# Optimization experiments

Hardware: AMD Instinct MI355X
Metric: run time of the kernel (lower is better)

The kernel has to match this reference:

```python
import jax, jax.numpy as jnp
import numpy as np

DT = 0.005


def quat_product(q, r):
    # q, r: [B, 4] -> [B, 4]
    q0, q1, q2, q3 = q[:, 0], q[:, 1], q[:, 2], q[:, 3]
    r0, r1, r2, r3 = r[:, 0], r[:, 1], r[:, 2], r[:, 3]
    return jnp.stack([
        q0 * r0 - q1 * r1 - q2 * r2 - q3 * r3,
        q0 * r1 + q1 * r0 + q2 * r3 - q3 * r2,
        q0 * r2 - q1 * r3 + q2 * r0 + q3 * r1,
        q0 * r3 + q1 * r2 - q2 * r1 + q3 * r0,
    ], axis=1)


def quat_rotate(q, v):
    # q: [B, 4], v: [B, 3] -> [B, 3]
    q_conj = jnp.concatenate([q[:, :1], -q[:, 1:]], axis=1)
    v_quat = jnp.concatenate([jnp.zeros_like(v[:, :1]), v], axis=1)
    return quat_product(quat_product(q, v_quat), q_conj)[:, 1:]


def setup_inputs() -> dict:
    key = jax.random.key(0)
    ks = jax.random.split(key, 8)
    B, S, F, N = 1048576, 10, 6, 2097152
    return {
        "true_quaternions": jax.random.normal(ks[0], (B, 4), dtype=jnp.float32),
        "true_positions": jax.random.normal(ks[1], (B, 3), dtype=jnp.float32),
        "predicted_biases": jax.random.normal(ks[2], (B, 3), dtype=jnp.float32),
        "batch_X": jax.random.normal(ks[3], (B, S, F), dtype=jnp.float32),
        "positions_all": jax.random.normal(ks[4], (N, 3), dtype=jnp.float32),
        "velocities_all": jax.random.normal(ks[5], (N, 3), dtype=jnp.float32),
        "gravity_vector": jnp.array([0.0, 0.0, -9.81], dtype=jnp.float32),
        "indices": jax.random.randint(ks[6], (B,), 0, N, dtype=jnp.int64 if jax.config.jax_enable_x64 else jnp.int32),
        "sequence_length": 10,
    }


def reference(true_quaternions, true_positions, predicted_biases, batch_X,
              positions_all, velocities_all, gravity_vector, indices,
              sequence_length):
    # gather initial state: initial_index = max(idx - (seq_len - 1), 0)
    init_idx = jnp.maximum(indices - (sequence_length - 1), 0)
    p0 = positions_all[init_idx]   # [B, 3]
    v0 = velocities_all[init_idx]  # [B, 3]
    # bias-corrected acceleration from last timestep (disturbance = 0)
    acc = batch_X[:, -1, 0:3] - predicted_biases  # [B, 3]
    rotated = 0.5 * quat_rotate(true_quaternions, acc) * DT ** 2
    pred = p0 + v0 * DT + 0.5 * gravity_vector * DT ** 2 + rotated
    # Huber loss, delta = 1.0; per-sample mean over 3 coords then batch mean
    # equals elementwise mean over all B*3 elements
    d = pred - true_positions
    ad = jnp.abs(d)
    h = jnp.where(ad < 1.0, 0.5 * d * d, ad - 0.5)
    return jnp.mean(h)
```

## Files before the change

### kernel.cpp

```cpp
#include <hip/hip_runtime.h>
#include <math.h>

#define DT 0.005f
#define NTHREADS 256
#define NBLOCKS 2048
#define NBUCKET 32
#define ELEMS_PER_BLOCK 1024
#define ROUNDS 4

typedef float    fvec4 __attribute__((ext_vector_type(4)));
typedef float    fvec2 __attribute__((ext_vector_type(2)));
typedef unsigned uvec4 __attribute__((ext_vector_type(4)));
typedef float    fvec4u __attribute__((ext_vector_type(4), aligned(4)));

__device__ __forceinline__ fvec4 ntload4f(const float* p) {
    return __builtin_nontemporal_load(reinterpret_cast<const fvec4*>(p));
}
__device__ __forceinline__ fvec2 ntload2f(const float* p) {
    return __builtin_nontemporal_load(reinterpret_cast<const fvec2*>(p));
}
__device__ __forceinline__ float ntloadf(const float* p) {
    return __builtin_nontemporal_load(p);
}
__device__ __forceinline__ int ntloadi(const int* p) {
    return __builtin_nontemporal_load(p);
}
__device__ __forceinline__ uvec4 ntload4u(const unsigned* p) {
    return __builtin_nontemporal_load(reinterpret_cast<const uvec4*>(p));
}

__device__ __forceinline__ void stream_compute(
    const float* __restrict__ quat, const float* __restrict__ tpos,
    const float* __restrict__ bias, const float* __restrict__ batchX,
    int i, int SF, int last_off,
    float gx, float gy, float gz, float half_dt2,
    float& cx, float& cy, float& cz)
{
    fvec4 q = ntload4f(quat + (size_t)i * 4);
    const float* tp = tpos + (size_t)i * 3;
    float tpx = ntloadf(tp + 0), tpy = ntloadf(tp + 1), tpz = ntloadf(tp + 2);
    const float* bp = bias + (size_t)i * 3;
    float bx = ntloadf(bp + 0), by = ntloadf(bp + 1), bz = ntloadf(bp + 2);
    const float* xb = batchX + (size_t)i * SF + last_off;
    fvec2 a01 = ntload2f(xb);
    float ax = a01.x - bx;
    float ay = a01.y - by;
    float az = ntloadf(xb + 2) - bz;

    float t0 = -(q.y * ax + q.z * ay + q.w * az);
    float t1 =   q.x * ax + q.z * az - q.w * ay;
    float t2 =   q.x * ay - q.y * az + q.w * ax;
    float t3 =   q.x * az + q.y * ay - q.z * ax;
    float rx = -t0 * q.y + t1 * q.x - t2 * q.w + t3 * q.z;
    float ry = -t0 * q.z + t1 * q.w + t2 * q.x - t3 * q.y;
    float rz = -t0 * q.w - t1 * q.z + t2 * q.y + t3 * q.x;

    cx = half_dt2 * (gx + rx) - tpx;
    cy = half_dt2 * (gy + ry) - tpy;
    cz = half_dt2 * (gz + rz) - tpz;
}

__device__ __forceinline__ float huber3(float dx, float dy, float dz) {
    float adx = fabsf(dx), ady = fabsf(dy), adz = fabsf(dz);
    float h = (adx < 1.f) ? 0.5f * dx * dx : adx - 0.5f;
    h += (ady < 1.f) ? 0.5f * dy * dy : ady - 0.5f;
    h += (adz < 1.f) ? 0.5f * dz * dz : adz - 0.5f;
    return h;
}

__global__ __launch_bounds__(NTHREADS) void k1_bin(
    const float* __restrict__ quat,
    const float* __restrict__ tpos,
    const float* __restrict__ bias,
    const float* __restrict__ batchX,
    const float* __restrict__ grav,
    const int*   __restrict__ indices,
    const int*   __restrict__ seq_len_p,
    int SF, int shift,
    uvec4* __restrict__ pairs,
    int*   __restrict__ dirs)
{
    const int S = *seq_len_p;
    const int F = SF / S;
    const int last_off = (S - 1) * F;
    const float gx = grav[0], gy = grav[1], gz = grav[2];
    const float half_dt2 = 0.5f * DT * DT;

    __shared__ int   cnt[ROUNDS][4][NBUCKET];
    __shared__ int   offarr[ROUNDS][4][NBUCKET];
    __shared__ int   bstart[NBUCKET];
    __shared__ uvec4 stage[ELEMS_PER_BLOCK];

    const int tid  = threadIdx.x;
    const int wave = tid >> 6;
    const int lane = tid & 63;
    const unsigned long long ltmask = (1ull << lane) - 1ull;

    for (int k = tid; k < ROUNDS * 4 * NBUCKET; k += NTHREADS)
        ((int*)cnt)[k] = 0;
    __syncthreads();

    const int base = blockIdx.x * ELEMS_PER_BLOCK;

    int   idxv[ROUNDS], bckt[ROUNDS], rnk[ROUNDS];
    float cxv[ROUNDS], cyv[ROUNDS], czv[ROUNDS];

    #pragma unroll
    for (int r = 0; r < ROUNDS; ++r) {
        const int i = base + r * NTHREADS + tid;
        int idx = ntloadi(indices + i) - (S - 1);
        if (idx < 0) idx = 0;
        idxv[r] = idx;
        int b = idx >> shift; if (b > NBUCKET - 1) b = NBUCKET - 1;
        bckt[r] = b;

        unsigned long long mask = ~0ull;
        #pragma unroll
        for (int k = 0; k < 5; ++k) {
            unsigned long long bm = __ballot((b >> k) & 1);
            mask &= ((b >> k) & 1) ? bm : ~bm;
        }
        rnk[r] = __popcll(mask & ltmask);
        if (rnk[r] == 0) cnt[r][wave][b] = __popcll(mask);

        stream_compute(quat, tpos, bias, batchX, i, SF, last_off,
                       gx, gy, gz, half_dt2, cxv[r], cyv[r], czv[r]);
    }
    __syncthreads();

    if (tid < NBUCKET) {
        int b = tid, off = 0;
        #pragma unroll
        for (int r = 0; r < ROUNDS; ++r)
            #pragma unroll
            for (int w = 0; w < 4; ++w) {
                offarr[r][w][b] = off;
                off += cnt[r][w][b];
            }
        dirs[blockIdx.x * NBUCKET + b] = off;
        cnt[0][0][b] = off;
    }
    __syncthreads();
    if (tid == 0) {
        int s = 0;
        #pragma unroll
        for (int b = 0; b < NBUCKET; ++b) { bstart[b] = s; s += cnt[0][0][b]; }
    }
    __syncthreads();

    #pragma unroll
    for (int r = 0; r < ROUNDS; ++r) {
        int slot = bstart[bckt[r]] + offarr[r][wave][bckt[r]] + rnk[r];
        uvec4 v;
        v.x = (unsigned)idxv[r];
        v.y = __float_as_uint(cxv[r]);
        v.z = __float_as_uint(cyv[r]);
        v.w = __float_as_uint(czv[r]);
        stage[slot] = v;
    }
    __syncthreads();

    #pragma unroll
    for (int r = 0; r < ROUNDS; ++r)
        pairs[(size_t)base + r * NTHREADS + tid] = stage[r * NTHREADS + tid];
}

__global__ __launch_bounds__(NTHREADS) void k2_gather(
    const float* __restrict__ pos_all,
    const float* __restrict__ vel_all,
    const uvec4* __restrict__ pairs,
    const int*   __restrict__ dirs,
    int Nm1,
    float* __restrict__ partials)
{
    const int r = blockIdx.x & 7;
    const int j = blockIdx.x >> 3;
    const int tid = threadIdx.x;

    __shared__ int dcnt[8][NBUCKET];
    __shared__ int segSrc[8];
    __shared__ int segCum[9];
    __shared__ float wsum[NTHREADS / 64];

    {
        int s = tid >> 5, bb = tid & (NBUCKET - 1);
        dcnt[s][bb] = dirs[(j * 8 + s) * NBUCKET + bb];
    }
    __syncthreads();

    float hsum = 0.f;

    for (int phase = 0; phase < NBUCKET / 8; ++phase) {
        const int b = r + 8 * phase;

        if (tid < 8) {
            int s = tid, st = 0;
            for (int bb = 0; bb < b; ++bb) st += dcnt[s][bb];
            segSrc[s] = (j * 8 + s) * ELEMS_PER_BLOCK + st;
            segCum[s] = dcnt[s][b];
        }
        __syncthreads();
        if (tid == 0) {
            int c = 0;
            #pragma unroll
            for (int s = 0; s < 8; ++s) { int l = segCum[s]; segCum[s] = c; c += l; }
            segCum[8] = c;
        }
        __syncthreads();

        const int tot = segCum[8];
        for (int m = tid; m < tot; m += NTHREADS) {
            int s = 0;
            #pragma unroll
            for (int k = 1; k < 8; ++k) s += (m >= segCum[k]);
            uvec4 pr = ntload4u(
                reinterpret_cast<const unsigned*>(pairs + segSrc[s] + (m - segCum[s])));
            int idx = (int)pr.x;

            float px, py, pz, vx, vy, vz;
            if (idx < Nm1) {
                fvec4u pv = *reinterpret_cast<const fvec4u*>(pos_all + (size_t)idx * 3);
                fvec4u vv = *reinterpret_cast<const fvec4u*>(vel_all + (size_t)idx * 3);
                px = pv.x; py = pv.y; pz = pv.z;
                vx = vv.x; vy = vv.y; vz = vv.z;
            } else {
                const float* pp = pos_all + (size_t)idx * 3;
                const float* vp = vel_all + (size_t)idx * 3;
                px = pp[0]; py = pp[1]; pz = pp[2];
                vx = vp[0]; vy = vp[1]; vz = vp[2];
            }

            hsum += huber3(px + vx * DT + __uint_as_float(pr.y),
                           py + vy * DT + __uint_as_float(pr.z),
                           pz + vz * DT + __uint_as_float(pr.w));
        }
        __syncthreads();
    }

    for (int off = 32; off > 0; off >>= 1)
        hsum += __shfl_down(hsum, off);

    int lane = tid & 63, wid = tid >> 6;
    if (lane == 0) wsum[wid] = hsum;
    __syncthreads();
    if (tid == 0) {
        float s = 0.f;
        for (int w = 0; w < NTHREADS / 64; ++w) s += wsum[w];
        partials[blockIdx.x] = s;
    }
}

__global__ __launch_bounds__(NTHREADS) void pos_loss_partial(
    const float* __restrict__ quat,
    const float* __restrict__ tpos,
    const float* __restrict__ bias,
    const float* __restrict__ batchX,
    const float* __restrict__ pos_all,
    const float* __restrict__ vel_all,
    const float* __restrict__ grav,
    const int*   __restrict__ indices,
    const int*   __restrict__ seq_len_p,
    int B, int SF,
    float* __restrict__ partials)
{
    const int S = *seq_len_p;
    const int F = SF / S;
    const int last_off = (S - 1) * F;
    const float gx = grav[0], gy = grav[1], gz = grav[2];
    const float half_dt2 = 0.5f * DT * DT;

    float hsum = 0.f;

    for (int i = blockIdx.x * blockDim.x + threadIdx.x; i < B;
         i += gridDim.x * blockDim.x) {
        int idx = ntloadi(indices + i) - (S - 1);
        if (idx < 0) idx = 0;
        const float* pp = pos_all + (size_t)idx * 3;
        const float* vp = vel_all + (size_t)idx * 3;
        float p0x = pp[0], p0y = pp[1], p0z = pp[2];
        float v0x = vp[0], v0y = vp[1], v0z = vp[2];

        float cx, cy, cz;
        stream_compute(quat, tpos, bias, batchX, i, SF, last_off,
                       gx, gy, gz, half_dt2, cx, cy, cz);

        hsum += huber3(p0x + v0x * DT + cx,
                       p0y + v0y * DT + cy,
                       p0z + v0z * DT + cz);
    }

    for (int off = 32; off > 0; off >>= 1)
        hsum += __shfl_down(hsum, off);

    __shared__ float wsum[NTHREADS / 64];
    int lane = threadIdx.x & 63;
    int wid  = threadIdx.x >> 6;
    if (lane == 0) wsum[wid] = hsum;
    __syncthreads();
    if (threadIdx.x == 0) {
        float s = 0.f;
        for (int w = 0; w < NTHREADS / 64; ++w) s += wsum[w];
        partials[blockIdx.x] = s;
    }
}

__global__ __launch_bounds__(NTHREADS) void pos_loss_finish(
    const float* __restrict__ partials, int nb, float inv_cnt,
    float* __restrict__ out)
{
    float s = 0.f;
    for (int i = threadIdx.x; i < nb; i += NTHREADS) s += partials[i];
    for (int off = 32; off > 0; off >>= 1)
        s += __shfl_down(s, off);
    __shared__ float wsum[NTHREADS / 64];
    int lane = threadIdx.x & 63;
    int wid  = threadIdx.x >> 6;
    if (lane == 0) wsum[wid] = s;
    __syncthreads();
    if (threadIdx.x == 0) {
        float tot = 0.f;
        for (int w = 0; w < NTHREADS / 64; ++w) tot += wsum[w];
        out[0] = tot * inv_cnt;
    }
}

extern "C" void kernel_launch(void* const* d_in, const int* in_sizes, int n_in,
                              void* d_out, int out_size, void* d_ws, size_t ws_size,
                              hipStream_t stream) {
    const float* quat    = (const float*)d_in[0];
    const float* tpos    = (const float*)d_in[1];
    const float* bias    = (const float*)d_in[2];
    const float* batchX  = (const float*)d_in[3];
    const float* pos_all = (const float*)d_in[4];
    const float* vel_all = (const float*)d_in[5];
    const float* grav    = (const float*)d_in[6];
    const int*   indices = (const int*)d_in[7];
    const int*   seqlen  = (const int*)d_in[8];

    const int B  = in_sizes[0] / 4;
    const int SF = in_sizes[3] / B;
    const int N  = in_sizes[4] / 3;

    float inv_cnt = (float)(1.0 / (3.0 * (double)B));
    float* outp = (float*)d_out;

    const int nseg = B / ELEMS_PER_BLOCK;
    uvec4* pairs    = (uvec4*)d_ws;
    int*   dirs     = (int*)((char*)d_ws + (size_t)B * 16);
    float* partials = (float*)((char*)d_ws + (size_t)B * 16 +
                               (size_t)nseg * NBUCKET * 4);
    const size_t need = (size_t)B * 16 + (size_t)nseg * NBUCKET * 4 +
                        (size_t)nseg * 4 + 256;

    const bool pipe_ok = (B % (ELEMS_PER_BLOCK * 8) == 0) && (ws_size >= need) &&
                         (N > NBUCKET);

    if (pipe_ok) {
        int shift = 0;
        while (((long long)(N - 1) >> shift) >= NBUCKET) ++shift;

        k1_bin<<<nseg, NTHREADS, 0, stream>>>(
            quat, tpos, bias, batchX, grav, indices, seqlen,
            SF, shift, pairs, dirs);
        k2_gather<<<nseg, NTHREADS, 0, stream>>>(
            pos_all, vel_all, pairs, dirs, N - 1, partials);
        pos_loss_finish<<<1, NTHREADS, 0, stream>>>(
            partials, nseg, inv_cnt, outp);
    } else {
        float* fpart = (float*)d_ws;
        pos_loss_partial<<<NBLOCKS, NTHREADS, 0, stream>>>(
            quat, tpos, bias, batchX, pos_all, vel_all, grav, indices, seqlen,
            B, SF, fpart);
        pos_loss_finish<<<1, NTHREADS, 0, stream>>>(
            fpart, NBLOCKS, inv_cnt, outp);
    }
}
```

Before: 59.73 us.

## Pack binned records into 8 bytes with fp16 offsets and fuse final reduction

The intermediate per-sample record written by the binning kernel and read by the gather kernel shrinks from 16 bytes to 8. It holds a 16-bit index relative to its bucket base and three fp16 partial-position terms. This halves that round-trip traffic, but the fp16 rounding of the offsets adds error to the loss. The final partial-sum reduction is folded into the gather kernel through a cooperative grid sync when occupancy allows, removing a separate launch. The batchX load also becomes a single unaligned 4-wide load.

```diff
diff --git a/kernel.cpp b/kernel.cpp
--- a/kernel.cpp
+++ b/kernel.cpp
@@ -1,4 +1,6 @@
 #include <hip/hip_runtime.h>
+#include <hip/hip_fp16.h>
+#include <hip/hip_cooperative_groups.h>
 #include <math.h>
 
 #define DT 0.005f
@@ -8,6 +10,8 @@
 #define ELEMS_PER_BLOCK 1024
 #define ROUNDS 4
 
+namespace cg = cooperative_groups;
+
 typedef float    fvec4 __attribute__((ext_vector_type(4)));
 typedef float    fvec2 __attribute__((ext_vector_type(2)));
 typedef unsigned uvec4 __attribute__((ext_vector_type(4)));
@@ -16,17 +20,21 @@
 __device__ __forceinline__ fvec4 ntload4f(const float* p) {
     return __builtin_nontemporal_load(reinterpret_cast<const fvec4*>(p));
 }
-__device__ __forceinline__ fvec2 ntload2f(const float* p) {
-    return __builtin_nontemporal_load(reinterpret_cast<const fvec2*>(p));
-}
 __device__ __forceinline__ float ntloadf(const float* p) {
     return __builtin_nontemporal_load(p);
 }
 __device__ __forceinline__ int ntloadi(const int* p) {
     return __builtin_nontemporal_load(p);
 }
-__device__ __forceinline__ uvec4 ntload4u(const unsigned* p) {
-    return __builtin_nontemporal_load(reinterpret_cast<const uvec4*>(p));
+__device__ __forceinline__ unsigned long long ntload8(const unsigned long long* p) {
+    return __builtin_nontemporal_load(p);
+}
+
+__device__ __forceinline__ unsigned short f2h(float f) {
+    return __half_as_ushort(__float2half(f));
+}
+__device__ __forceinline__ float h2f(unsigned short u) {
+    return __half2float(__ushort_as_half(u));
 }
 
 __device__ __forceinline__ void stream_compute(
@@ -42,10 +50,10 @@
     const float* bp = bias + (size_t)i * 3;
     float bx = ntloadf(bp + 0), by = ntloadf(bp + 1), bz = ntloadf(bp + 2);
     const float* xb = batchX + (size_t)i * SF + last_off;
-    fvec2 a01 = ntload2f(xb);
-    float ax = a01.x - bx;
-    float ay = a01.y - by;
-    float az = ntloadf(xb + 2) - bz;
+    fvec4u a = *reinterpret_cast<const fvec4u*>(xb);
+    float ax = a.x - bx;
+    float ay = a.y - by;
+    float az = a.z - bz;
 
     float t0 = -(q.y * ax + q.z * ay + q.w * az);
     float t1 =   q.x * ax + q.z * az - q.w * ay;
@@ -77,7 +85,7 @@
     const int*   __restrict__ indices,
     const int*   __restrict__ seq_len_p,
     int SF, int shift,
-    uvec4* __restrict__ pairs,
+    unsigned long long* __restrict__ pairs8,
     int*   __restrict__ dirs)
 {
     const int S = *seq_len_p;
@@ -89,7 +97,7 @@
     __shared__ int   cnt[ROUNDS][4][NBUCKET];
     __shared__ int   offarr[ROUNDS][4][NBUCKET];
     __shared__ int   bstart[NBUCKET];
-    __shared__ uvec4 stage[ELEMS_PER_BLOCK];
+    __shared__ unsigned long long stage[ELEMS_PER_BLOCK];
 
     const int tid  = threadIdx.x;
     const int wave = tid >> 6;
@@ -151,27 +159,29 @@
     #pragma unroll
     for (int r = 0; r < ROUNDS; ++r) {
         int slot = bstart[bckt[r]] + offarr[r][wave][bckt[r]] + rnk[r];
-        uvec4 v;
-        v.x = (unsigned)idxv[r];
-        v.y = __float_as_uint(cxv[r]);
-        v.z = __float_as_uint(cyv[r]);
-        v.w = __float_as_uint(czv[r]);
-        stage[slot] = v;
+        unsigned long long e =
+            (unsigned long long)((unsigned)(idxv[r] - (bckt[r] << shift)) & 0xFFFFu)
+          | ((unsigned long long)f2h(cxv[r]) << 16)
+          | ((unsigned long long)f2h(cyv[r]) << 32)
+          | ((unsigned long long)f2h(czv[r]) << 48);
+        stage[slot] = e;
     }
     __syncthreads();
 
     #pragma unroll
     for (int r = 0; r < ROUNDS; ++r)
-        pairs[(size_t)base + r * NTHREADS + tid] = stage[r * NTHREADS + tid];
-}
-
+        pairs8[(size_t)base + r * NTHREADS + tid] = stage[r * NTHREADS + tid];
+}
+
+template <bool FUSE>
 __global__ __launch_bounds__(NTHREADS) void k2_gather(
     const float* __restrict__ pos_all,
     const float* __restrict__ vel_all,
-    const uvec4* __restrict__ pairs,
+    const unsigned long long* __restrict__ pairs8,
     const int*   __restrict__ dirs,
-    int Nm1,
-    float* __restrict__ partials)
+    int shift, int Nm1, int nseg, float inv_cnt,
+    float* __restrict__ partials,
+    float* __restrict__ out)
 {
     const int r = blockIdx.x & 7;
     const int j = blockIdx.x >> 3;
@@ -192,6 +202,7 @@
 
     for (int phase = 0; phase < NBUCKET / 8; ++phase) {
         const int b = r + 8 * phase;
+        const int bbase = b << shift;
 
         if (tid < 8) {
             int s = tid, st = 0;
@@ -213,9 +224,8 @@
             int s = 0;
             #pragma unroll
             for (int k = 1; k < 8; ++k) s += (m >= segCum[k]);
-            uvec4 pr = ntload4u(
-                reinterpret_cast<const unsigned*>(pairs + segSrc[s] + (m - segCum[s])));
-            int idx = (int)pr.x;
+            unsigned long long e = ntload8(pairs8 + segSrc[s] + (m - segCum[s]));
+            int idx = bbase + (int)(e & 0xFFFFull);
 
             float px, py, pz, vx, vy, vz;
             if (idx < Nm1) {
@@ -230,9 +240,9 @@
                 vx = vp[0]; vy = vp[1]; vz = vp[2];
             }
 
-            hsum += huber3(px + vx * DT + __uint_as_float(pr.y),
-                           py + vy * DT + __uint_as_float(pr.z),
-                           pz + vz * DT + __uint_as_float(pr.w));
+            hsum += huber3(px + vx * DT + h2f((unsigned short)(e >> 16)),
+                           py + vy * DT + h2f((unsigned short)(e >> 32)),
+                           pz + vz * DT + h2f((unsigned short)(e >> 48)));
         }
         __syncthreads();
     }
@@ -247,6 +257,25 @@
         float s = 0.f;
         for (int w = 0; w < NTHREADS / 64; ++w) s += wsum[w];
         partials[blockIdx.x] = s;
+    }
+
+    if constexpr (FUSE) {
+        __threadfence();
+        cg::this_grid().sync();
+        if (blockIdx.x == 0) {
+            float s = 0.f;
+            for (int i = tid; i < nseg; i += NTHREADS) s += partials[i];
+            for (int off = 32; off > 0; off >>= 1)
+                s += __shfl_down(s, off);
+            __syncthreads();
+            if (lane == 0) wsum[wid] = s;
+            __syncthreads();
+            if (tid == 0) {
+                float tot = 0.f;
+                for (int w = 0; w < NTHREADS / 64; ++w) tot += wsum[w];
+                out[0] = tot * inv_cnt;
+            }
+        }
     }
 }
 
@@ -280,13 +309,29 @@
         float p0x = pp[0], p0y = pp[1], p0z = pp[2];
         float v0x = vp[0], v0y = vp[1], v0z = vp[2];
 
-        float cx, cy, cz;
-        stream_compute(quat, tpos, bias, batchX, i, SF, last_off,
-                       gx, gy, gz, half_dt2, cx, cy, cz);
-
-        hsum += huber3(p0x + v0x * DT + cx,
-                       p0y + v0y * DT + cy,
-                       p0z + v0z * DT + cz);
+        fvec4 q = ntload4f(quat + (size_t)i * 4);
+        const float* tp = tpos + (size_t)i * 3;
+        float tpx = ntloadf(tp + 0), tpy = ntloadf(tp + 1), tpz = ntloadf(tp + 2);
+        const float* bp = bias + (size_t)i * 3;
+        float bx = ntloadf(bp + 0), by = ntloadf(bp + 1), bz = ntloadf(bp + 2);
+        const float* xb = batchX + (size_t)i * SF + last_off;
+        float ax = ntloadf(xb + 0) - bx;
+        float ay = ntloadf(xb + 1) - by;
+        float az = ntloadf(xb + 2) - bz;
+
+        float t0 = -(q.y * ax + q.z * ay + q.w * az);
+        float t1 =   q.x * ax + q.z * az - q.w * ay;
+        float t2 =   q.x * ay - q.y * az + q.w * ax;
+        float t3 =   q.x * az + q.y * ay - q.z * ax;
+        float rx = -t0 * q.y + t1 * q.x - t2 * q.w + t3 * q.z;
+        float ry = -t0 * q.z + t1 * q.w + t2 * q.x - t3 * q.y;
+        float rz = -t0 * q.w - t1 * q.z + t2 * q.y + t3 * q.x;
+
+        float px = p0x + v0x * DT + half_dt2 * (gx + rx);
+        float py = p0y + v0y * DT + half_dt2 * (gy + ry);
+        float pz = p0z + v0z * DT + half_dt2 * (gz + rz);
+
+        hsum += huber3(px - tpx, py - tpy, pz - tpz);
     }
 
     for (int off = 32; off > 0; off >>= 1)
@@ -345,25 +390,52 @@
     float* outp = (float*)d_out;
 
     const int nseg = B / ELEMS_PER_BLOCK;
-    uvec4* pairs    = (uvec4*)d_ws;
-    int*   dirs     = (int*)((char*)d_ws + (size_t)B * 16);
-    float* partials = (float*)((char*)d_ws + (size_t)B * 16 +
+    unsigned long long* pairs8 = (unsigned long long*)d_ws;
+    int*   dirs     = (int*)((char*)d_ws + (size_t)B * 8);
+    float* partials = (float*)((char*)d_ws + (size_t)B * 8 +
                                (size_t)nseg * NBUCKET * 4);
-    const size_t need = (size_t)B * 16 + (size_t)nseg * NBUCKET * 4 +
+    const size_t need = (size_t)B * 8 + (size_t)nseg * NBUCKET * 4 +
                         (size_t)nseg * 4 + 256;
 
+    int shift = 0;
+    while (((long long)(N - 1) >> shift) >= NBUCKET) ++shift;
+
     const bool pipe_ok = (B % (ELEMS_PER_BLOCK * 8) == 0) && (ws_size >= need) &&
-                         (N > NBUCKET);
+                         (N > NBUCKET) && (shift <= 16);
 
     if (pipe_ok) {
-        int shift = 0;
-        while (((long long)(N - 1) >> shift) >= NBUCKET) ++shift;
-
         k1_bin<<<nseg, NTHREADS, 0, stream>>>(
             quat, tpos, bias, batchX, grav, indices, seqlen,
-            SF, shift, pairs, dirs);
-        k2_gather<<<nseg, NTHREADS, 0, stream>>>(
-            pos_all, vel_all, pairs, dirs, N - 1, partials);
+            SF, shift, pairs8, dirs);
+
+        bool coop_ok = true;
+        int dev = 0;
+        hipGetDevice(&dev);
+        int coop_attr = 0;
+        hipDeviceGetAttribute(&coop_attr, hipDeviceAttributeCooperativeLaunch, dev);
+        int num_cu = 0;
+        hipDeviceGetAttribute(&num_cu, hipDeviceAttributeMultiprocessorCount, dev);
+        int max_blk = 0;
+        hipOccupancyMaxActiveBlocksPerMultiprocessor(&max_blk, k2_gather<true>,
+                                                     NTHREADS, 0);
+        coop_ok = coop_attr && (max_blk * num_cu >= nseg);
+
+        if (coop_ok) {
+            int Nm1 = N - 1;
+            void* args[] = {
+                (void*)&pos_all, (void*)&vel_all, (void*)&pairs8, (void*)&dirs,
+                (void*)&shift, (void*)&Nm1, (void*)&nseg, (void*)&inv_cnt,
+                (void*)&partials, (void*)&outp
+            };
+            hipError_t err = hipLaunchCooperativeKernel(
+                (const void*)k2_gather<true>, dim3(nseg), dim3(NTHREADS),
+                args, 0, stream);
+            if (err == hipSuccess) return;
+        }
+
+        k2_gather<false><<<nseg, NTHREADS, 0, stream>>>(
+            pos_all, vel_all, pairs8, dirs, shift, N - 1, nseg, inv_cnt,
+            partials, outp);
         pos_loss_finish<<<1, NTHREADS, 0, stream>>>(
             partials, nseg, inv_cnt, outp);
     } else {
```

Result: slower. 233.4 us (+290.7%).
